# Kernel tuning notes

Measured on AMD Instinct MI355X. Metric: run time of the kernel, lower is better.

Reference implementation:

```python
import jax, jax.numpy as jnp
import numpy as np

EPS = 1e-6


def _mlp(x, W1, b1, W2, b2):
    # x: [b,s]; W1: [m,s,h]; W2: [m,h,o] -> [m,b,o]  (m = stacked module dim)
    h = jnp.tanh(jnp.einsum('bs,msh->mbh', x, W1) + b1[:, None, :])
    return jnp.einsum('mbh,mho->mbo', h, W2) + b2[:, None, :]


def _ln(x, g, b):
    mu = jnp.mean(x, axis=-1, keepdims=True)
    var = jnp.var(x, axis=-1, keepdims=True)
    return g * (x - mu) / jnp.sqrt(var + EPS) + b


def setup_inputs() -> dict:
    B, S, H, E, R, L = 1024, 256, 512, 64, 32, 9
    key = jax.random.key(0)
    ks = jax.random.split(key, 8)

    def xavier(k, shape):
        bound = np.sqrt(6.0 / (shape[-2] + shape[-1])).astype(np.float32)
        return jax.random.uniform(k, shape, jnp.float32, -bound, bound)

    return {
        'query_embed': jax.random.normal(ks[0], (B, S), jnp.float32),
        'tpr': jax.random.normal(ks[1], (B, E, R, E), jnp.float32) * 0.1,
        'eW1': xavier(ks[2], (2, S, H)), 'eb1': jnp.zeros((2, H), jnp.float32),
        'eW2': xavier(ks[3], (2, H, E)), 'eb2': jnp.zeros((2, E), jnp.float32),
        'rW1': xavier(ks[4], (3, S, H)), 'rb1': jnp.zeros((3, H), jnp.float32),
        'rW2': xavier(ks[5], (3, H, R)), 'rb2': jnp.zeros((3, R), jnp.float32),
        'ln_g': jnp.ones((3, E), jnp.float32), 'ln_b': jnp.zeros((3, E), jnp.float32),
        'Z': xavier(ks[6], (E, L)),
    }


def reference(query_embed, tpr, eW1, eb1, eW2, eb2, rW1, rb1, rW2, rb2, ln_g, ln_b, Z):
    e = _mlp(query_embed, eW1, eb1, eW2, eb2)   # [2,B,E] (e[1] unused, as in original)
    r = _mlp(query_embed, rW1, rb1, rW2, rb2)   # [3,B,R]
    i1 = _ln(jnp.einsum('be,br,berf->bf', e[0], r[0], tpr), ln_g[0], ln_b[0])
    i2 = _ln(jnp.einsum('be,br,berf->bf', i1, r[1], tpr), ln_g[1], ln_b[1])
    i3 = _ln(jnp.einsum('be,br,berf->bf', i2, r[2], tpr), ln_g[2], ln_b[2])
    step_sum = i1 + i2 + i3
    return jnp.einsum('bf,fl->bl', step_sum, Z)
```

## Files before the change

### kernel.cpp

```cpp
#include <hip/hip_runtime.h>
#include <math.h>

#define B_  1024
#define S_  256
#define H_  512
#define E_  64
#define R_  32
#define L_  9
#define EPS_ 1e-6f
#define TB  8

__global__ __launch_bounds__(256) void mlp_kernel(
    const float* __restrict__ x,
    const float* __restrict__ eW1, const float* __restrict__ eb1,
    const float* __restrict__ eW2, const float* __restrict__ eb2,
    const float* __restrict__ rW1, const float* __restrict__ rb1,
    const float* __restrict__ rW2, const float* __restrict__ rb2,
    float* __restrict__ e0_out,
    float* __restrict__ r_out)
{
    __shared__ __align__(16) float xs[TB][S_];
    __shared__ __align__(16) float hs[TB][H_];
    const int t  = threadIdx.x;
    const int b0 = blockIdx.x * TB;
    const int m  = blockIdx.y;

    {
        const float4* x4 = (const float4*)(x + (size_t)b0 * S_);
        float4* xs4 = (float4*)&xs[0][0];
        xs4[t]       = x4[t];
        xs4[t + 256] = x4[t + 256];
    }
    __syncthreads();

    const float* W1 = (m == 0) ? eW1 : (rW1 + (size_t)(m - 1) * S_ * H_);
    const float* b1 = (m == 0) ? eb1 : (rb1 + (size_t)(m - 1) * H_);

    float acc0[TB], acc1[TB];
    #pragma unroll
    for (int bb = 0; bb < TB; ++bb) { acc0[bb] = 0.0f; acc1[bb] = 0.0f; }

    for (int s4 = 0; s4 < S_ / 4; ++s4) {
        const float* Wp = W1 + (size_t)(4 * s4) * H_ + t;
        float wa0 = Wp[0];          float wb0 = Wp[256];
        float wa1 = Wp[H_];         float wb1 = Wp[H_ + 256];
        float wa2 = Wp[2 * H_];     float wb2 = Wp[2 * H_ + 256];
        float wa3 = Wp[3 * H_];     float wb3 = Wp[3 * H_ + 256];
        #pragma unroll
        for (int bb = 0; bb < TB; ++bb) {
            float4 xv = ((const float4*)&xs[bb][0])[s4];
            acc0[bb] = fmaf(xv.x, wa0, acc0[bb]);
            acc1[bb] = fmaf(xv.x, wb0, acc1[bb]);
            acc0[bb] = fmaf(xv.y, wa1, acc0[bb]);
            acc1[bb] = fmaf(xv.y, wb1, acc1[bb]);
            acc0[bb] = fmaf(xv.z, wa2, acc0[bb]);
            acc1[bb] = fmaf(xv.z, wb2, acc1[bb]);
            acc0[bb] = fmaf(xv.w, wa3, acc0[bb]);
            acc1[bb] = fmaf(xv.w, wb3, acc1[bb]);
        }
    }
    float bias0 = b1[t], bias1 = b1[t + 256];
    #pragma unroll
    for (int bb = 0; bb < TB; ++bb) {
        hs[bb][t]       = tanhf(acc0[bb] + bias0);
        hs[bb][t + 256] = tanhf(acc1[bb] + bias1);
    }
    __syncthreads();

    if (m == 0) {
        const float* W2 = eW2;
        const float* b2 = eb2;
        int o  = t & 63;
        int bq = t >> 6;
        #pragma unroll
        for (int i = 0; i < TB / 4; ++i) {
            int bb = bq + i * 4;
            float a0 = 0.f, a1 = 0.f, a2 = 0.f, a3 = 0.f;
            #pragma unroll 4
            for (int j = 0; j < H_; j += 4) {
                float4 hv = ((const float4*)&hs[bb][0])[j >> 2];
                a0 = fmaf(hv.x, W2[(size_t)(j + 0) * E_ + o], a0);
                a1 = fmaf(hv.y, W2[(size_t)(j + 1) * E_ + o], a1);
                a2 = fmaf(hv.z, W2[(size_t)(j + 2) * E_ + o], a2);
                a3 = fmaf(hv.w, W2[(size_t)(j + 3) * E_ + o], a3);
            }
            e0_out[(size_t)(b0 + bb) * E_ + o] = b2[o] + ((a0 + a1) + (a2 + a3));
        }
    } else {
        const float* W2 = rW2 + (size_t)(m - 1) * H_ * R_;
        const float* b2 = rb2 + (size_t)(m - 1) * R_;
        int o  = t & 31;
        int bb = t >> 5;
        float a0 = 0.f, a1 = 0.f, a2 = 0.f, a3 = 0.f;
        #pragma unroll 4
        for (int j = 0; j < H_; j += 4) {
            float4 hv = ((const float4*)&hs[bb][0])[j >> 2];
            a0 = fmaf(hv.x, W2[(size_t)(j + 0) * R_ + o], a0);
            a1 = fmaf(hv.y, W2[(size_t)(j + 1) * R_ + o], a1);
            a2 = fmaf(hv.z, W2[(size_t)(j + 2) * R_ + o], a2);
            a3 = fmaf(hv.w, W2[(size_t)(j + 3) * R_ + o], a3);
        }
        r_out[((size_t)(m - 1) * B_ + (b0 + bb)) * R_ + o] = b2[o] + ((a0 + a1) + (a2 + a3));
    }
}

__global__ __launch_bounds__(256) void tpr_kernel(
    const float* __restrict__ tpr,
    const float* __restrict__ e0,
    const float* __restrict__ rws,
    const float* __restrict__ ln_g,
    const float* __restrict__ ln_b,
    const float* __restrict__ Z,
    float* __restrict__ out)
{
    __shared__ __align__(16) float M[2][E_][E_];
    __shared__ __align__(16) float red[4][E_];
    __shared__ float xcur[E_];
    __shared__ float ssum_sh[E_];
    __shared__ float rsh[3][R_];
    __shared__ float e0sh[E_];

    const int t = threadIdx.x;
    const int b = blockIdx.x;

    if (t < 96) { int k = t >> 5, j = t & 31; rsh[k][j] = rws[((size_t)k * B_ + b) * R_ + j]; }
    if (t < E_) e0sh[t] = e0[(size_t)b * E_ + t];
    __syncthreads();

    const int w  = t >> 6;
    const int j  = t & 63;
    const int jh = j >> 4;
    const float4* base = (const float4*)(tpr + (size_t)b * E_ * R_ * E_) + w * 8192;

    float wk0[8], wk1[8], wk2[8];
    #pragma unroll
    for (int it = 0; it < 8; ++it) {
        int r = it * 4 + jh;
        wk0[it] = rsh[0][r]; wk1[it] = rsh[1][r]; wk2[it] = rsh[2][r];
    }

    float4 t0p = {0, 0, 0, 0};
    for (int el = 0; el < 16; ++el) {
        float4 a0 = {0,0,0,0}, a1 = {0,0,0,0}, a2 = {0,0,0,0};
        #pragma unroll
        for (int it = 0; it < 8; ++it) {
            float4 v = base[el * 512 + it * 64 + j];
            float w0 = wk0[it], w1 = wk1[it], w2 = wk2[it];
            a0.x = fmaf(w0, v.x, a0.x); a0.y = fmaf(w0, v.y, a0.y);
            a0.z = fmaf(w0, v.z, a0.z); a0.w = fmaf(w0, v.w, a0.w);
            a1.x = fmaf(w1, v.x, a1.x); a1.y = fmaf(w1, v.y, a1.y);
            a1.z = fmaf(w1, v.z, a1.z); a1.w = fmaf(w1, v.w, a1.w);
            a2.x = fmaf(w2, v.x, a2.x); a2.y = fmaf(w2, v.y, a2.y);
            a2.z = fmaf(w2, v.z, a2.z); a2.w = fmaf(w2, v.w, a2.w);
        }
        #pragma unroll
        for (int st = 16; st <= 32; st <<= 1) {
            a0.x += __shfl_xor(a0.x, st); a0.y += __shfl_xor(a0.y, st);
            a0.z += __shfl_xor(a0.z, st); a0.w += __shfl_xor(a0.w, st);
            a1.x += __shfl_xor(a1.x, st); a1.y += __shfl_xor(a1.y, st);
            a1.z += __shfl_xor(a1.z, st); a1.w += __shfl_xor(a1.w, st);
            a2.x += __shfl_xor(a2.x, st); a2.y += __shfl_xor(a2.y, st);
            a2.z += __shfl_xor(a2.z, st); a2.w += __shfl_xor(a2.w, st);
        }
        const int e = w * 16 + el;
        if (j < 16) {
            ((float4*)&M[0][e][0])[j] = a1;
            ((float4*)&M[1][e][0])[j] = a2;
        }
        float ev = e0sh[e];
        t0p.x = fmaf(ev, a0.x, t0p.x); t0p.y = fmaf(ev, a0.y, t0p.y);
        t0p.z = fmaf(ev, a0.z, t0p.z); t0p.w = fmaf(ev, a0.w, t0p.w);
    }
    if (j < 16) ((float4*)&red[w][0])[j] = t0p;
    __syncthreads();

    if (t < E_) {
        const int f = t;
        float acc = 0.0f;
        #pragma unroll
        for (int g = 0; g < 4; ++g) acc += red[g][f];

        float ssum = 0.0f;
        #pragma unroll
        for (int k = 0; k < 3; ++k) {
            float s = acc;
            #pragma unroll
            for (int off = 32; off >= 1; off >>= 1) s += __shfl_xor(s, off, 64);
            float mu = s * (1.0f / 64.0f);
            float d = acc - mu;
            float vs = d * d;
            #pragma unroll
            for (int off = 32; off >= 1; off >>= 1) vs += __shfl_xor(vs, off, 64);
            float var = vs * (1.0f / 64.0f);
            float iv = ln_g[k * E_ + f] * d * rsqrtf(var + EPS_) + ln_b[k * E_ + f];
            ssum += iv;
            if (k < 2) {
                xcur[f] = iv;
                float n0 = 0.f, n1 = 0.f, n2 = 0.f, n3 = 0.f;
                #pragma unroll 4
                for (int e = 0; e < E_; e += 4) {
                    n0 = fmaf(xcur[e + 0], M[k][e + 0][f], n0);
                    n1 = fmaf(xcur[e + 1], M[k][e + 1][f], n1);
                    n2 = fmaf(xcur[e + 2], M[k][e + 2][f], n2);
                    n3 = fmaf(xcur[e + 3], M[k][e + 3][f], n3);
                }
                acc = (n0 + n1) + (n2 + n3);
            }
        }
        ssum_sh[f] = ssum;

        if (t < L_) {
            float o = 0.0f;
            #pragma unroll
            for (int f2 = 0; f2 < E_; ++f2)
                o = fmaf(ssum_sh[f2], Z[f2 * L_ + t], o);
            out[(size_t)b * L_ + t] = o;
        }
    }
}

extern "C" void kernel_launch(void* const* d_in, const int* in_sizes, int n_in,
                              void* d_out, int out_size, void* d_ws, size_t ws_size,
                              hipStream_t stream) {
    const float* x    = (const float*)d_in[0];
    const float* tpr  = (const float*)d_in[1];
    const float* eW1  = (const float*)d_in[2];
    const float* eb1  = (const float*)d_in[3];
    const float* eW2  = (const float*)d_in[4];
    const float* eb2  = (const float*)d_in[5];
    const float* rW1  = (const float*)d_in[6];
    const float* rb1  = (const float*)d_in[7];
    const float* rW2  = (const float*)d_in[8];
    const float* rb2  = (const float*)d_in[9];
    const float* ln_g = (const float*)d_in[10];
    const float* ln_b = (const float*)d_in[11];
    const float* Z    = (const float*)d_in[12];
    float* out = (float*)d_out;

    float* e0_ws = (float*)d_ws;
    float* r_ws  = e0_ws + (size_t)B_ * E_;

    dim3 g1(B_ / TB, 4);
    mlp_kernel<<<g1, 256, 0, stream>>>(x, eW1, eb1, eW2, eb2,
                                       rW1, rb1, rW2, rb2, e0_ws, r_ws);
    tpr_kernel<<<B_, 256, 0, stream>>>(tpr, e0_ws, r_ws, ln_g, ln_b, Z, out);
}
```

Before: 748.1 us.

## Vectorize MLP weight loads and double-buffer TPR row loads

The first MLP layer now has each thread load float4 weight vectors covering four adjacent hidden units and accumulate for four batch rows, instead of scalar loads for two hidden units across eight rows. The TPR contraction loop now uses register double-buffering, issuing the next row's global loads before consuming the current row so memory latency overlaps with FMA and shuffle work. The cost is higher register pressure from two 8-entry float4 buffers, which could reduce occupancy.

```diff
diff --git a/kernel.cpp b/kernel.cpp
--- a/kernel.cpp
+++ b/kernel.cpp
@@ -36,34 +36,43 @@
     const float* W1 = (m == 0) ? eW1 : (rW1 + (size_t)(m - 1) * S_ * H_);
     const float* b1 = (m == 0) ? eb1 : (rb1 + (size_t)(m - 1) * H_);
 
-    float acc0[TB], acc1[TB];
+    const int c4   = t & 127;
+    const int half = t >> 7;
+
+    float4 acc[4];
     #pragma unroll
-    for (int bb = 0; bb < TB; ++bb) { acc0[bb] = 0.0f; acc1[bb] = 0.0f; }
+    for (int q = 0; q < 4; ++q) acc[q] = (float4){0, 0, 0, 0};
 
     for (int s4 = 0; s4 < S_ / 4; ++s4) {
-        const float* Wp = W1 + (size_t)(4 * s4) * H_ + t;
-        float wa0 = Wp[0];          float wb0 = Wp[256];
-        float wa1 = Wp[H_];         float wb1 = Wp[H_ + 256];
-        float wa2 = Wp[2 * H_];     float wb2 = Wp[2 * H_ + 256];
-        float wa3 = Wp[3 * H_];     float wb3 = Wp[3 * H_ + 256];
-        #pragma unroll
-        for (int bb = 0; bb < TB; ++bb) {
-            float4 xv = ((const float4*)&xs[bb][0])[s4];
-            acc0[bb] = fmaf(xv.x, wa0, acc0[bb]);
-            acc1[bb] = fmaf(xv.x, wb0, acc1[bb]);
-            acc0[bb] = fmaf(xv.y, wa1, acc0[bb]);
-            acc1[bb] = fmaf(xv.y, wb1, acc1[bb]);
-            acc0[bb] = fmaf(xv.z, wa2, acc0[bb]);
-            acc1[bb] = fmaf(xv.z, wb2, acc1[bb]);
-            acc0[bb] = fmaf(xv.w, wa3, acc0[bb]);
-            acc1[bb] = fmaf(xv.w, wb3, acc1[bb]);
-        }
-    }
-    float bias0 = b1[t], bias1 = b1[t + 256];
-    #pragma unroll
-    for (int bb = 0; bb < TB; ++bb) {
-        hs[bb][t]       = tanhf(acc0[bb] + bias0);
-        hs[bb][t + 256] = tanhf(acc1[bb] + bias1);
+        const float4* Wrow = (const float4*)(W1 + (size_t)(4 * s4) * H_);
+        float4 w0 = Wrow[c4];
+        float4 w1 = Wrow[128 + c4];
+        float4 w2 = Wrow[256 + c4];
+        float4 w3 = Wrow[384 + c4];
+        #pragma unroll
+        for (int q = 0; q < 4; ++q) {
+            float4 xv = ((const float4*)&xs[half * 4 + q][0])[s4];
+            acc[q].x = fmaf(xv.x, w0.x, acc[q].x); acc[q].y = fmaf(xv.x, w0.y, acc[q].y);
+            acc[q].z = fmaf(xv.x, w0.z, acc[q].z); acc[q].w = fmaf(xv.x, w0.w, acc[q].w);
+            acc[q].x = fmaf(xv.y, w1.x, acc[q].x); acc[q].y = fmaf(xv.y, w1.y, acc[q].y);
+            acc[q].z = fmaf(xv.y, w1.z, acc[q].z); acc[q].w = fmaf(xv.y, w1.w, acc[q].w);
+            acc[q].x = fmaf(xv.z, w2.x, acc[q].x); acc[q].y = fmaf(xv.z, w2.y, acc[q].y);
+            acc[q].z = fmaf(xv.z, w2.z, acc[q].z); acc[q].w = fmaf(xv.z, w2.w, acc[q].w);
+            acc[q].x = fmaf(xv.w, w3.x, acc[q].x); acc[q].y = fmaf(xv.w, w3.y, acc[q].y);
+            acc[q].z = fmaf(xv.w, w3.z, acc[q].z); acc[q].w = fmaf(xv.w, w3.w, acc[q].w);
+        }
+    }
+    {
+        float4 bias4 = ((const float4*)b1)[c4];
+        #pragma unroll
+        for (int q = 0; q < 4; ++q) {
+            float4 hv;
+            hv.x = tanhf(acc[q].x + bias4.x);
+            hv.y = tanhf(acc[q].y + bias4.y);
+            hv.z = tanhf(acc[q].z + bias4.z);
+            hv.w = tanhf(acc[q].w + bias4.w);
+            ((float4*)&hs[half * 4 + q][0])[c4] = hv;
+        }
     }
     __syncthreads();
 
@@ -139,38 +148,58 @@
         wk0[it] = rsh[0][r]; wk1[it] = rsh[1][r]; wk2[it] = rsh[2][r];
     }
 
+#define LOADROW(BUF, EL)                                                   \
+    {                                                                      \
+        _Pragma("unroll")                                                  \
+        for (int it = 0; it < 8; ++it)                                     \
+            BUF[it] = base[(EL) * 512 + it * 64 + j];                      \
+    }
+
+#define CONSUME(BUF, EL)                                                   \
+    {                                                                      \
+        float4 a0 = {0,0,0,0}, a1 = {0,0,0,0}, a2 = {0,0,0,0};             \
+        _Pragma("unroll")                                                  \
+        for (int it = 0; it < 8; ++it) {                                   \
+            float4 v = BUF[it];                                            \
+            float w0 = wk0[it], w1 = wk1[it], w2 = wk2[it];                 \
+            a0.x = fmaf(w0, v.x, a0.x); a0.y = fmaf(w0, v.y, a0.y);        \
+            a0.z = fmaf(w0, v.z, a0.z); a0.w = fmaf(w0, v.w, a0.w);        \
+            a1.x = fmaf(w1, v.x, a1.x); a1.y = fmaf(w1, v.y, a1.y);        \
+            a1.z = fmaf(w1, v.z, a1.z); a1.w = fmaf(w1, v.w, a1.w);        \
+            a2.x = fmaf(w2, v.x, a2.x); a2.y = fmaf(w2, v.y, a2.y);        \
+            a2.z = fmaf(w2, v.z, a2.z); a2.w = fmaf(w2, v.w, a2.w);        \
+        }                                                                  \
+        _Pragma("unroll")                                                  \
+        for (int st = 16; st <= 32; st <<= 1) {                            \
+            a0.x += __shfl_xor(a0.x, st); a0.y += __shfl_xor(a0.y, st);    \
+            a0.z += __shfl_xor(a0.z, st); a0.w += __shfl_xor(a0.w, st);    \
+            a1.x += __shfl_xor(a1.x, st); a1.y += __shfl_xor(a1.y, st);    \
+            a1.z += __shfl_xor(a1.z, st); a1.w += __shfl_xor(a1.w, st);    \
+            a2.x += __shfl_xor(a2.x, st); a2.y += __shfl_xor(a2.y, st);    \
+            a2.z += __shfl_xor(a2.z, st); a2.w += __shfl_xor(a2.w, st);    \
+        }                                                                  \
+        const int e = w * 16 + (EL);                                       \
+        if (j < 16) {                                                      \
+            ((float4*)&M[0][e][0])[j] = a1;                                \
+            ((float4*)&M[1][e][0])[j] = a2;                                \
+        }                                                                  \
+        float ev = e0sh[e];                                                \
+        t0p.x = fmaf(ev, a0.x, t0p.x); t0p.y = fmaf(ev, a0.y, t0p.y);      \
+        t0p.z = fmaf(ev, a0.z, t0p.z); t0p.w = fmaf(ev, a0.w, t0p.w);      \
+    }
+
     float4 t0p = {0, 0, 0, 0};
-    for (int el = 0; el < 16; ++el) {
-        float4 a0 = {0,0,0,0}, a1 = {0,0,0,0}, a2 = {0,0,0,0};
-        #pragma unroll
-        for (int it = 0; it < 8; ++it) {
-            float4 v = base[el * 512 + it * 64 + j];
-            float w0 = wk0[it], w1 = wk1[it], w2 = wk2[it];
-            a0.x = fmaf(w0, v.x, a0.x); a0.y = fmaf(w0, v.y, a0.y);
-            a0.z = fmaf(w0, v.z, a0.z); a0.w = fmaf(w0, v.w, a0.w);
-            a1.x = fmaf(w1, v.x, a1.x); a1.y = fmaf(w1, v.y, a1.y);
-            a1.z = fmaf(w1, v.z, a1.z); a1.w = fmaf(w1, v.w, a1.w);
-            a2.x = fmaf(w2, v.x, a2.x); a2.y = fmaf(w2, v.y, a2.y);
-            a2.z = fmaf(w2, v.z, a2.z); a2.w = fmaf(w2, v.w, a2.w);
-        }
-        #pragma unroll
-        for (int st = 16; st <= 32; st <<= 1) {
-            a0.x += __shfl_xor(a0.x, st); a0.y += __shfl_xor(a0.y, st);
-            a0.z += __shfl_xor(a0.z, st); a0.w += __shfl_xor(a0.w, st);
-            a1.x += __shfl_xor(a1.x, st); a1.y += __shfl_xor(a1.y, st);
-            a1.z += __shfl_xor(a1.z, st); a1.w += __shfl_xor(a1.w, st);
-            a2.x += __shfl_xor(a2.x, st); a2.y += __shfl_xor(a2.y, st);
-            a2.z += __shfl_xor(a2.z, st); a2.w += __shfl_xor(a2.w, st);
-        }
-        const int e = w * 16 + el;
-        if (j < 16) {
-            ((float4*)&M[0][e][0])[j] = a1;
-            ((float4*)&M[1][e][0])[j] = a2;
-        }
-        float ev = e0sh[e];
-        t0p.x = fmaf(ev, a0.x, t0p.x); t0p.y = fmaf(ev, a0.y, t0p.y);
-        t0p.z = fmaf(ev, a0.z, t0p.z); t0p.w = fmaf(ev, a0.w, t0p.w);
-    }
+    float4 bA[8], bB[8];
+    LOADROW(bA, 0);
+    for (int el = 0; el < 16; el += 2) {
+        LOADROW(bB, el + 1);
+        CONSUME(bA, el);
+        if (el + 2 < 16) LOADROW(bA, el + 2);
+        CONSUME(bB, el + 1);
+    }
+#undef LOADROW
+#undef CONSUME
+
     if (j < 16) ((float4*)&red[w][0])[j] = t0p;
     __syncthreads();
 
```

Result: no change. 753.7 us (+0.7%).
